# Performance work log

Hardware: AMD Instinct MI355X
Metric: run time of the kernel (lower is better)

The kernel has to match this reference:

```python
import jax, jax.numpy as jnp
import numpy as np

B, N, K = 8, 8192, 48
NUM_POS = 16
NUM_FREQ = NUM_POS // 2
NUM_EDGE = 16
EPS = 1e-12


def l2norm(x, axis=-1):
    # torch F.normalize: x / max(||x||_2, eps)
    return x / jnp.maximum(jnp.linalg.norm(x, axis=axis, keepdims=True), EPS)


def setup_inputs() -> dict:
    key = jax.random.key(0)
    k1, k2, k3, k4 = jax.random.split(key, 4)
    p = jax.random.normal(k1, (B, N, 3), dtype=jnp.float32) * 3.0
    e_idx = jax.random.randint(k2, (B, N, K), 0, N)
    mask = jnp.ones((B, N), dtype=jnp.float32)
    # LRPE params
    t_frq = jnp.exp(jax.random.normal(k3, (NUM_FREQ,), dtype=jnp.float32)) * (-np.log(10000.0) / NUM_POS)
    t_s = jnp.array(1.0, dtype=jnp.float32)
    # edge_embedding: Linear(NUM_POS + 7, NUM_EDGE)
    fan_in = NUM_POS + 7
    W = jax.random.uniform(k4, (NUM_EDGE, fan_in), minval=-1.0, maxval=1.0, dtype=jnp.float32) / np.sqrt(fan_in)
    b = jnp.zeros((NUM_EDGE,), dtype=jnp.float32)
    return {"p": p, "e_idx": e_idx, "mask": mask, "t_frq": t_frq, "t_s": t_s, "W": W, "b": b}


def _quaternions(R):
    # R: [B,N,K,3,3] -> Q: [B,N,K,4]
    diag = jnp.diagonal(R, axis1=-2, axis2=-1)  # [B,N,K,3]
    Rxx, Ryy, Rzz = diag[..., 0], diag[..., 1], diag[..., 2]
    mags = 0.5 * jnp.sqrt(jnp.abs(1.0 + jnp.stack(
        [Rxx - Ryy - Rzz, -Rxx + Ryy - Rzz, -Rxx - Ryy + Rzz], axis=-1)) + EPS)
    signs = jnp.sign(jnp.stack(
        [R[..., 2, 1] - R[..., 1, 2],
         R[..., 0, 2] - R[..., 2, 0],
         R[..., 1, 0] - R[..., 0, 1]], axis=-1))
    xyz = signs * mags
    w = jnp.sqrt(jax.nn.relu(1.0 + jnp.sum(diag, axis=-1, keepdims=True)) + EPS) / 2.0
    Q = jnp.concatenate((xyz, w), axis=-1)
    return l2norm(Q, axis=-1)


def _orientations(X, E_idx):
    # X: [B,N,3], E_idx: [B,N,K]
    dX = X[:, 1:, :] - X[:, :-1, :]
    U = l2norm(dX)                       # [B,N-1,3]
    u_2 = U[:, :-2, :]
    u_1 = U[:, 1:-1, :]
    n_2 = l2norm(jnp.cross(u_2, u_1))
    o_1 = l2norm(u_2 - u_1)
    O = jnp.stack((o_1, n_2, jnp.cross(o_1, n_2)), axis=2)  # [B,N-3,3,3]
    O = O.reshape(O.shape[0], O.shape[1], 9)
    O = jnp.pad(O, ((0, 0), (1, 2), (0, 0)))                # [B,N,9]

    bidx = jnp.arange(X.shape[0])[:, None, None]
    O_nb = O[bidx, E_idx]                # [B,N,K,9]
    X_nb = X[bidx, E_idx]                # [B,N,K,3]

    Of = O.reshape(O.shape[0], O.shape[1], 3, 3)            # [B,N,3,3]
    O_nb = O_nb.reshape(O_nb.shape[0], O_nb.shape[1], O_nb.shape[2], 3, 3)

    dXn = X_nb - X[:, :, None, :]        # [B,N,K,3]
    dU = l2norm(jnp.einsum('bnij,bnkj->bnki', Of, dXn))     # O @ dX
    R = jnp.einsum('bnji,bnkjl->bnkil', Of, O_nb)           # O^T @ O_nb
    Q = _quaternions(R)
    return jnp.concatenate((dU, Q), axis=-1)  # [B,N,K,7]


def _lrpe(e_idx, t_frq, t_s):
    num_nodes = e_idx.shape[1]
    ii = jnp.arange(num_nodes, dtype=jnp.float32).reshape(1, -1, 1)
    d = (e_idx.astype(jnp.float32) - ii)[..., None]         # [B,N,K,1]
    FR = t_frq * t_s
    angles = d * FR.reshape(1, 1, 1, -1)                    # [B,N,K,NUM_FREQ]
    return jnp.concatenate((jnp.sin(angles), jnp.cos(angles)), axis=-1)


def reference(p, e_idx, mask, t_frq, t_s, W, b):
    # eval mode: no noise augmentation (mask unused)
    q_feats = _orientations(p, e_idx)                       # [B,N,K,7]
    e_pe = _lrpe(e_idx, t_frq, t_s)                         # [B,N,K,16]
    e_cat = jnp.concatenate((e_pe, q_feats), axis=-1)       # [B,N,K,23]
    h_e = jnp.einsum('bnkf,of->bnko', e_cat, W) + b         # [B,N,K,16]
    # torch F.normalize default dim=1 -> normalize along node dim
    return l2norm(h_e, axis=1)
```

## Files before the change

### kernel.cpp

```cpp
#include <hip/hip_runtime.h>
#include <math.h>

constexpr int B_ = 8;
constexpr int N_ = 8192;
constexpr int K_ = 48;
constexpr int NFREQ = 8;
constexpr int NEDGE = 16;
constexpr int FANIN = 23;
constexpr float EPSF = 1e-12f;
constexpr int DRANGE = 2 * N_ - 1;

struct F3 { float x, y, z; };
__device__ inline F3 f3(float a, float b, float c) { F3 r{a,b,c}; return r; }
__device__ inline F3 sub3(F3 a, F3 b) { return f3(a.x-b.x, a.y-b.y, a.z-b.z); }
__device__ inline F3 cross3(F3 a, F3 b) {
    return f3(a.y*b.z - a.z*b.y, a.z*b.x - a.x*b.z, a.x*b.y - a.y*b.x);
}
__device__ inline F3 norm3(F3 a) {
    float n = sqrtf(a.x*a.x + a.y*a.y + a.z*a.z);
    float inv = 1.0f / fmaxf(n, EPSF);
    return f3(a.x*inv, a.y*inv, a.z*inv);
}
__device__ inline float signf0(float x) {
    return (x > 0.0f) ? 1.0f : ((x < 0.0f) ? -1.0f : 0.0f);
}
__device__ inline unsigned int bf16rne(float x) {
    unsigned int u = __float_as_uint(x);
    return (u + 0x7fffu + ((u >> 16) & 1u)) >> 16;
}
__device__ inline void unpack8(uint4 v, float* f) {
    f[0] = __uint_as_float(v.x << 16); f[1] = __uint_as_float(v.x & 0xffff0000u);
    f[2] = __uint_as_float(v.y << 16); f[3] = __uint_as_float(v.y & 0xffff0000u);
    f[4] = __uint_as_float(v.z << 16); f[5] = __uint_as_float(v.z & 0xffff0000u);
    f[6] = __uint_as_float(v.w << 16); f[7] = __uint_as_float(v.w & 0xffff0000u);
}

__global__ void build_table(const float* __restrict__ tfrq, const float* __restrict__ ts,
                            const float* __restrict__ W, const float* __restrict__ bias,
                            unsigned short* __restrict__ T) {
    int idx = blockIdx.x * blockDim.x + threadIdx.x;
    if (idx >= DRANGE) return;
    float d = (float)(idx - (N_ - 1));
    float h[NEDGE];
    #pragma unroll
    for (int o = 0; o < NEDGE; o++) h[o] = bias[o];
    float tscale = ts[0];
    for (int f = 0; f < NFREQ; f++) {
        float s, c;
        sincosf(d * (tfrq[f] * tscale), &s, &c);
        #pragma unroll
        for (int o = 0; o < NEDGE; o++)
            h[o] = fmaf(s, W[o * FANIN + f], fmaf(c, W[o * FANIN + NFREQ + f], h[o]));
    }
    uint4 r0, r1;
    r0.x = bf16rne(h[0])  | (bf16rne(h[1])  << 16);
    r0.y = bf16rne(h[2])  | (bf16rne(h[3])  << 16);
    r0.z = bf16rne(h[4])  | (bf16rne(h[5])  << 16);
    r0.w = bf16rne(h[6])  | (bf16rne(h[7])  << 16);
    r1.x = bf16rne(h[8])  | (bf16rne(h[9])  << 16);
    r1.y = bf16rne(h[10]) | (bf16rne(h[11]) << 16);
    r1.z = bf16rne(h[12]) | (bf16rne(h[13]) << 16);
    r1.w = bf16rne(h[14]) | (bf16rne(h[15]) << 16);
    uint4* Tp = (uint4*)(T + (size_t)idx * 16);
    Tp[0] = r0; Tp[1] = r1;
}

__global__ void compute_F(const float* __restrict__ X, float* __restrict__ F) {
    int idx = blockIdx.x * blockDim.x + threadIdx.x;
    if (idx >= B_ * N_) return;
    int n = idx & (N_ - 1);
    const float* Xp = X + (size_t)idx * 3;
    float o[12];
    o[0] = Xp[0]; o[1] = Xp[1]; o[2] = Xp[2];
    #pragma unroll
    for (int i = 3; i < 12; i++) o[i] = 0.0f;
    if (n != 0 && n < N_ - 2) {
        F3 xm = f3(Xp[-3], Xp[-2], Xp[-1]);
        F3 x0 = f3(Xp[0], Xp[1], Xp[2]);
        F3 xp = f3(Xp[3], Xp[4], Xp[5]);
        F3 u2 = norm3(sub3(x0, xm));
        F3 u1 = norm3(sub3(xp, x0));
        F3 n2 = norm3(cross3(u2, u1));
        F3 o1 = norm3(sub3(u2, u1));
        F3 cc = cross3(o1, n2);
        o[3] = o1.x; o[4] = o1.y; o[5] = o1.z;
        o[6] = n2.x; o[7] = n2.y; o[8] = n2.z;
        o[9] = cc.x; o[10] = cc.y; o[11] = cc.z;
    }
    float4* Fp = (float4*)(F + (size_t)idx * 16);
    Fp[0] = make_float4(o[0], o[1], o[2], o[3]);
    Fp[1] = make_float4(o[4], o[5], o[6], o[7]);
    Fp[2] = make_float4(o[8], o[9], o[10], o[11]);
}

__device__ inline void compute_edge(float4 a0, float4 a1, float4 a2,
                                    const float* __restrict__ F,
                                    const unsigned short* __restrict__ T,
                                    const float (*sWq)[8],
                                    size_t bbase, int n, int j,
                                    float* __restrict__ h) {
    const float4* fjp = (const float4*)(F + (bbase + (size_t)j) * 16);
    float4 b0 = fjp[0], b1 = fjp[1], b2 = fjp[2];
    const uint4* tp = (const uint4*)(T + (size_t)(j - n + (N_ - 1)) * 16);
    uint4 t0 = tp[0], t1 = tp[1];
    float tv[16];
    unpack8(t0, tv);
    unpack8(t1, tv + 8);

    float A1x = a0.w, A1y = a1.x, A1z = a1.y;
    float A2x = a1.z, A2y = a1.w, A2z = a2.x;
    float A3x = a2.y, A3y = a2.z, A3z = a2.w;
    float B1x = b0.w, B1y = b1.x, B1z = b1.y;
    float B2x = b1.z, B2y = b1.w, B2z = b2.x;
    float B3x = b2.y, B3y = b2.z, B3z = b2.w;

    float dX0 = b0.x - a0.x, dX1 = b0.y - a0.y, dX2 = b0.z - a0.z;
    float v0 = A1x*dX0 + A1y*dX1 + A1z*dX2;
    float v1 = A2x*dX0 + A2y*dX1 + A2z*dX2;
    float v2 = A3x*dX0 + A3y*dX1 + A3z*dX2;
    float vinv = 1.0f / fmaxf(sqrtf(v0*v0 + v1*v1 + v2*v2), EPSF);
    float dU0 = v0*vinv, dU1 = v1*vinv, dU2 = v2*vinv;

    float R00 = A1x*B1x + A2x*B2x + A3x*B3x;
    float R11 = A1y*B1y + A2y*B2y + A3y*B3y;
    float R22 = A1z*B1z + A2z*B2z + A3z*B3z;
    float R21 = A1z*B1y + A2z*B2y + A3z*B3y;
    float R12 = A1y*B1z + A2y*B2z + A3y*B3z;
    float R02 = A1x*B1z + A2x*B2z + A3x*B3z;
    float R20 = A1z*B1x + A2z*B2x + A3z*B3x;
    float R10 = A1y*B1x + A2y*B2x + A3y*B3x;
    float R01 = A1x*B1y + A2x*B2y + A3x*B3y;

    float mg0 = 0.5f * sqrtf(fabsf(1.0f + R00 - R11 - R22) + EPSF);
    float mg1 = 0.5f * sqrtf(fabsf(1.0f - R00 + R11 - R22) + EPSF);
    float mg2 = 0.5f * sqrtf(fabsf(1.0f - R00 - R11 + R22) + EPSF);
    float qx = signf0(R21 - R12) * mg0;
    float qy = signf0(R02 - R20) * mg1;
    float qz = signf0(R10 - R01) * mg2;
    float qw = 0.5f * sqrtf(fmaxf(1.0f + R00 + R11 + R22, 0.0f) + EPSF);
    float qinv = 1.0f / fmaxf(sqrtf(qx*qx + qy*qy + qz*qz + qw*qw), EPSF);
    qx *= qinv; qy *= qinv; qz *= qinv; qw *= qinv;

    float q[7] = {dU0, dU1, dU2, qx, qy, qz, qw};
    #pragma unroll
    for (int o = 0; o < NEDGE; o++) {
        float a = tv[o];
        #pragma unroll
        for (int f = 0; f < 7; f++) a = fmaf(q[f], sWq[o][f], a);
        h[o] = a;
    }
}

__launch_bounds__(256, 8)
__global__ void edge_pass(const int* __restrict__ E, const float* __restrict__ F,
                          const unsigned short* __restrict__ T, const float* __restrict__ Wfull,
                          float* __restrict__ acc, float* __restrict__ out) {
    int bid = blockIdx.x;
    int b = bid & 7;
    int r = bid >> 3;
    int kg = r % 3;
    int nt = r / 3;
    int tid = threadIdx.x;
    int w = tid >> 6, l = tid & 63;
    int nn = l >> 4, kk = l & 15;
    int k = kg * 16 + kk;

    __shared__ float sT[4][64 * 17];
    __shared__ float sWq[NEDGE][8];
    __shared__ float sAcc[4][16][NEDGE];

    if (tid < NEDGE * 8) {
        int o = tid >> 3, f = tid & 7;
        sWq[o][f] = (f < 7) ? Wfull[o * FANIN + 16 + f] : 0.0f;
    }
    __syncthreads();

    size_t bbase = (size_t)b * N_;
    int nbase = nt * 64;
    float* myT = sT[w];

    float vsq[NEDGE];
    #pragma unroll
    for (int o = 0; o < NEDGE; o++) vsq[o] = 0.0f;

    for (int it = 0; it < 4; it++) {
        int n = nbase + it * 16 + w * 4 + nn;
        size_t node = bbase + n;
        const float4* fnp = (const float4*)(F + node * 16);
        float4 a0 = fnp[0], a1 = fnp[1], a2 = fnp[2];
        int j = E[node * K_ + k];

        float h[NEDGE];
        compute_edge(a0, a1, a2, F, T, sWq, bbase, n, j, h);

        #pragma unroll
        for (int o = 0; o < NEDGE; o++) vsq[o] = fmaf(h[o], h[o], vsq[o]);

        #pragma unroll
        for (int q = 0; q < 4; q++)
            *(float4*)(myT + l * 17 + q * 4) =
                make_float4(h[4*q], h[4*q+1], h[4*q+2], h[4*q+3]);

        #pragma unroll
        for (int s = 0; s < 4; s++) {
            int n_s = nbase + it * 16 + w * 4 + s;
            float4 v = *(float4*)(myT + ((s << 4) + (l >> 2)) * 17 + (l & 3) * 4);
            size_t outb = ((bbase + n_s) * K_ + kg * 16) * 16;
            *(float4*)(out + outb + l * 4) = v;
        }
    }

    #pragma unroll
    for (int o = 0; o < NEDGE; o++) {
        float v = vsq[o];
        v += __shfl_xor(v, 16, 64);
        v += __shfl_xor(v, 32, 64);
        vsq[o] = v;
    }
    if (nn == 0 && l < 16) {
        #pragma unroll
        for (int o = 0; o < NEDGE; o++) sAcc[w][kk][o] = vsq[o];
    }
    __syncthreads();
    {
        int kk2 = tid >> 4, o = tid & 15;
        float t = sAcc[0][kk2][o] + sAcc[1][kk2][o] + sAcc[2][kk2][o] + sAcc[3][kk2][o];
        atomicAdd(&acc[((size_t)b * K_ + kg * 16 + kk2) * NEDGE + o], t);
    }
}

__global__ void inv_kernel(const float* __restrict__ acc, float* __restrict__ rinv) {
    int i = blockIdx.x * blockDim.x + threadIdx.x;
    if (i >= B_ * K_ * NEDGE) return;
    rinv[i] = 1.0f / fmaxf(sqrtf(acc[i]), EPSF);
}

__launch_bounds__(256)
__global__ void scale_kernel(float* __restrict__ out, const float* __restrict__ rinv) {
    size_t idx = (size_t)blockIdx.x * blockDim.x + threadIdx.x;
    constexpr size_t TOTAL4 = (size_t)B_ * N_ * K_ * 4;
    if (idx >= TOTAL4) return;
    size_t e0 = idx * 4;
    unsigned int o0 = (unsigned int)(e0 & 15);
    unsigned int key = (unsigned int)(e0 >> 4);
    unsigned int k = key % (unsigned int)K_;
    unsigned int b = key / (unsigned int)(N_ * K_);
    const float* rp = rinv + ((size_t)b * K_ + k) * 16 + o0;
    float4 vv = *reinterpret_cast<float4*>(out + e0);
    vv.x *= rp[0]; vv.y *= rp[1]; vv.z *= rp[2]; vv.w *= rp[3];
    *reinterpret_cast<float4*>(out + e0) = vv;
}

extern "C" void kernel_launch(void* const* d_in, const int* in_sizes, int n_in,
                              void* d_out, int out_size, void* d_ws, size_t ws_size,
                              hipStream_t stream) {
    const float* X    = (const float*)d_in[0];
    const int*   E    = (const int*)d_in[1];
    const float* tfrq = (const float*)d_in[3];
    const float* ts   = (const float*)d_in[4];
    const float* W    = (const float*)d_in[5];
    const float* bias = (const float*)d_in[6];
    float* out = (float*)d_out;

    float* F = (float*)d_ws;
    unsigned short* T = (unsigned short*)(F + (size_t)B_ * N_ * 16);
    float* acc  = (float*)(T + (size_t)DRANGE * 16);
    float* rinv = acc + B_ * K_ * NEDGE;

    hipMemsetAsync(acc, 0, (size_t)B_ * K_ * NEDGE * sizeof(float), stream);

    build_table<<<(DRANGE + 255) / 256, 256, 0, stream>>>(tfrq, ts, W, bias, T);
    compute_F<<<(B_ * N_ + 255) / 256, 256, 0, stream>>>(X, F);

    int grid = 8 * 3 * 128;
    edge_pass<<<grid, 256, 0, stream>>>(E, F, T, W, acc, out);

    inv_kernel<<<(B_ * K_ * NEDGE + 255) / 256, 256, 0, stream>>>(acc, rinv);

    constexpr size_t TOTAL4 = (size_t)B_ * N_ * K_ * 4;
    scale_kernel<<<(TOTAL4 + 255) / 256, 256, 0, stream>>>(out, rinv);
}
```

Measured before the change: 147.0 us.

## Stage unnormalized edge features as bf16 scratch before the normalization pass

The edge pass now writes unnormalized outputs to a bf16 scratch buffer instead of fp32 output. A new scale kernel reads the bf16 values, applies the per-(b,k,o) inverse norm and writes fp32 output with nontemporal stores. This cuts intermediate write and read traffic roughly in half compared with the fp32 read-modify-write on the output, at the cost of bf16 rounding on every output value. The path is chosen only when the workspace holds the extra ~100MB of scratch.

New measurement: 224.5 us. 1.53x slower.

```diff
diff --git a/kernel.cpp b/kernel.cpp
--- a/kernel.cpp
+++ b/kernel.cpp
@@ -9,6 +9,8 @@
 constexpr int FANIN = 23;
 constexpr float EPSF = 1e-12f;
 constexpr int DRANGE = 2 * N_ - 1;
+
+typedef float f32x4 __attribute__((ext_vector_type(4)));
 
 struct F3 { float x, y, z; };
 __device__ inline F3 f3(float a, float b, float c) { F3 r{a,b,c}; return r; }
@@ -151,10 +153,12 @@
     }
 }
 
+template<bool BF16OUT>
 __launch_bounds__(256, 8)
 __global__ void edge_pass(const int* __restrict__ E, const float* __restrict__ F,
                           const unsigned short* __restrict__ T, const float* __restrict__ Wfull,
-                          float* __restrict__ acc, float* __restrict__ out) {
+                          float* __restrict__ acc, float* __restrict__ out,
+                          unsigned short* __restrict__ scr) {
     int bid = blockIdx.x;
     int b = bid & 7;
     int r = bid >> 3;
@@ -201,12 +205,32 @@
             *(float4*)(myT + l * 17 + q * 4) =
                 make_float4(h[4*q], h[4*q+1], h[4*q+2], h[4*q+3]);
 
-        #pragma unroll
-        for (int s = 0; s < 4; s++) {
-            int n_s = nbase + it * 16 + w * 4 + s;
-            float4 v = *(float4*)(myT + ((s << 4) + (l >> 2)) * 17 + (l & 3) * 4);
-            size_t outb = ((bbase + n_s) * K_ + kg * 16) * 16;
-            *(float4*)(out + outb + l * 4) = v;
+        if constexpr (BF16OUT) {
+            #pragma unroll
+            for (int s = 0; s < 2; s++) {
+                int rrow = (l >> 5) + 2 * s;
+                int e2   = (l & 31) >> 1;
+                int half = l & 1;
+                const float* src = myT + (((rrow << 4) | e2) * 17) + half * 8;
+                float4 v0 = *(const float4*)(src);
+                float4 v1 = *(const float4*)(src + 4);
+                uint4 p;
+                p.x = bf16rne(v0.x) | (bf16rne(v0.y) << 16);
+                p.y = bf16rne(v0.z) | (bf16rne(v0.w) << 16);
+                p.z = bf16rne(v1.x) | (bf16rne(v1.y) << 16);
+                p.w = bf16rne(v1.z) | (bf16rne(v1.w) << 16);
+                int n_s = nbase + it * 16 + w * 4 + rrow;
+                size_t scrb = ((bbase + n_s) * K_ + (size_t)kg * 16) * 16;
+                *(uint4*)(scr + scrb + (size_t)(l & 31) * 8) = p;
+            }
+        } else {
+            #pragma unroll
+            for (int s = 0; s < 4; s++) {
+                int n_s = nbase + it * 16 + w * 4 + s;
+                float4 v = *(float4*)(myT + ((s << 4) + (l >> 2)) * 17 + (l & 3) * 4);
+                size_t outb = ((bbase + n_s) * K_ + (size_t)kg * 16) * 16;
+                *(float4*)(out + outb + l * 4) = v;
+            }
         }
     }
 
@@ -233,6 +257,31 @@
     int i = blockIdx.x * blockDim.x + threadIdx.x;
     if (i >= B_ * K_ * NEDGE) return;
     rinv[i] = 1.0f / fmaxf(sqrtf(acc[i]), EPSF);
+}
+
+__launch_bounds__(256)
+__global__ void scale_bf16(const unsigned short* __restrict__ scr,
+                           const float* __restrict__ rinv, float* __restrict__ out) {
+    size_t e = (size_t)blockIdx.x * blockDim.x + threadIdx.x;
+    constexpr size_t TOTE = (size_t)B_ * N_ * K_;
+    if (e >= TOTE) return;
+    unsigned int k = (unsigned int)(e % (size_t)K_);
+    unsigned int b = (unsigned int)(e / ((size_t)N_ * K_));
+    const uint4* sp = (const uint4*)(scr + e * 16);
+    uint4 r0 = sp[0], r1 = sp[1];
+    float hv[16];
+    unpack8(r0, hv);
+    unpack8(r1, hv + 8);
+    const float* rp = rinv + ((size_t)b * K_ + k) * 16;
+    f32x4* op = (f32x4*)(out + e * 16);
+    f32x4 o0 = {hv[0]*rp[0],   hv[1]*rp[1],   hv[2]*rp[2],   hv[3]*rp[3]};
+    f32x4 o1 = {hv[4]*rp[4],   hv[5]*rp[5],   hv[6]*rp[6],   hv[7]*rp[7]};
+    f32x4 o2 = {hv[8]*rp[8],   hv[9]*rp[9],   hv[10]*rp[10], hv[11]*rp[11]};
+    f32x4 o3 = {hv[12]*rp[12], hv[13]*rp[13], hv[14]*rp[14], hv[15]*rp[15]};
+    __builtin_nontemporal_store(o0, op + 0);
+    __builtin_nontemporal_store(o1, op + 1);
+    __builtin_nontemporal_store(o2, op + 2);
+    __builtin_nontemporal_store(o3, op + 3);
 }
 
 __launch_bounds__(256)
@@ -266,17 +315,26 @@
     unsigned short* T = (unsigned short*)(F + (size_t)B_ * N_ * 16);
     float* acc  = (float*)(T + (size_t)DRANGE * 16);
     float* rinv = acc + B_ * K_ * NEDGE;
-
-    hipMemsetAsync(acc, 0, (size_t)B_ * K_ * NEDGE * sizeof(float), stream);
+    unsigned short* scr = (unsigned short*)(rinv + B_ * K_ * NEDGE);
+
+    constexpr size_t NEED = 4194304 + 524256 + 24576 + 24576 + 100663296;
+    const bool use_bf16 = (ws_size >= NEED);
+
+    (void)hipMemsetAsync(acc, 0, (size_t)B_ * K_ * NEDGE * sizeof(float), stream);
 
     build_table<<<(DRANGE + 255) / 256, 256, 0, stream>>>(tfrq, ts, W, bias, T);
     compute_F<<<(B_ * N_ + 255) / 256, 256, 0, stream>>>(X, F);
 
     int grid = 8 * 3 * 128;
-    edge_pass<<<grid, 256, 0, stream>>>(E, F, T, W, acc, out);
-
-    inv_kernel<<<(B_ * K_ * NEDGE + 255) / 256, 256, 0, stream>>>(acc, rinv);
-
-    constexpr size_t TOTAL4 = (size_t)B_ * N_ * K_ * 4;
-    scale_kernel<<<(TOTAL4 + 255) / 256, 256, 0, stream>>>(out, rinv);
-}
+    if (use_bf16) {
+        edge_pass<true><<<grid, 256, 0, stream>>>(E, F, T, W, acc, out, scr);
+        inv_kernel<<<(B_ * K_ * NEDGE + 255) / 256, 256, 0, stream>>>(acc, rinv);
+        constexpr size_t TOTE = (size_t)B_ * N_ * K_;
+        scale_bf16<<<(int)((TOTE + 255) / 256), 256, 0, stream>>>(scr, rinv, out);
+    } else {
+        edge_pass<false><<<grid, 256, 0, stream>>>(E, F, T, W, acc, out, scr);
+        inv_kernel<<<(B_ * K_ * NEDGE + 255) / 256, 256, 0, stream>>>(acc, rinv);
+        constexpr size_t TOTAL4 = (size_t)B_ * N_ * K_ * 4;
+        scale_kernel<<<(int)((TOTAL4 + 255) / 256), 256, 0, stream>>>(out, rinv);
+    }
+}
```
